# Optimization experiments

Hardware: AMD Instinct MI355X
Metric: run time of the kernel (lower is better)

The kernel has to match this reference:

```python
import jax, jax.numpy as jnp
import numpy as np

WIN = (4, 4, 4)
SHIFT = (2, 2, 2)
HEADS = 6


def _rel_index(win):
    H, W, D = win
    coords = np.stack(np.meshgrid(np.arange(H), np.arange(W), np.arange(D), indexing='ij'))
    cf = coords.reshape(3, -1)
    rel = (cf[:, :, None] - cf[:, None, :]).transpose(1, 2, 0)
    rel[..., 0] += H - 1
    rel[..., 1] += W - 1
    rel[..., 2] += D - 1
    rel[..., 0] *= (2 * W - 1) * (2 * D - 1)
    rel[..., 1] *= 2 * D - 1
    return rel.sum(-1)  # [N, N] int


def _attn_mask(shape, win, shift):
    H, W, D = shape
    wh, ww, wd = win
    mask = np.zeros((H, W, D))
    cnt = 0
    for h in (slice(0, -wh), slice(-wh, -shift[0]), slice(-shift[0], None)):
        for w in (slice(0, -ww), slice(-ww, -shift[1]), slice(-shift[1], None)):
            for d in (slice(0, -wd), slice(-wd, -shift[2]), slice(-shift[2], None)):
                mask[h, w, d] = cnt
                cnt += 1
    m = mask.reshape(H // wh, wh, W // ww, ww, D // wd, wd)
    m = m.transpose(0, 2, 4, 1, 3, 5).reshape(-1, wh * ww * wd)  # [nW, N]
    am = m[:, None, :] - m[:, :, None]
    return np.where(am != 0, -100.0, 0.0).astype(np.float32)  # [nW, N, N]


def _win_part(x, win):
    B, H, W, D, C = x.shape
    wh, ww, wd = win
    x = x.reshape(B, H // wh, wh, W // ww, ww, D // wd, wd, C)
    x = x.transpose(0, 1, 3, 5, 2, 4, 6, 7)
    return x.reshape(-1, wh * ww * wd, C)


def _win_rev(wins, win, shape):
    B, H, W, D, C = shape
    wh, ww, wd = win
    x = wins.reshape(B, H // wh, W // ww, D // wd, wh, ww, wd, C)
    x = x.transpose(0, 1, 4, 2, 5, 3, 6, 7)
    return x.reshape(B, H, W, D, C)


def _ln(x, g, b):
    m = x.mean(-1, keepdims=True)
    v = ((x - m) ** 2).mean(-1, keepdims=True)
    return (x - m) / jnp.sqrt(v + 1e-5) * g + b


def setup_inputs() -> dict:
    key = jax.random.key(0)
    ks = jax.random.split(key, 8)
    C, Hd = 192, 768
    s = 0.02
    return {
        'x': jax.random.normal(ks[0], (2, 32, 32, 32, C), jnp.float32),
        'g1': jnp.ones((C,), jnp.float32),
        'b1': jnp.zeros((C,), jnp.float32),
        'wqkv': jax.random.normal(ks[1], (C, 3 * C), jnp.float32) * s,
        'bqkv': jnp.zeros((3 * C,), jnp.float32),
        'wo': jax.random.normal(ks[2], (C, C), jnp.float32) * s,
        'bo': jnp.zeros((C,), jnp.float32),
        'bias_table': jax.random.normal(ks[3], (343, HEADS), jnp.float32) * s,
        'g2': jnp.ones((C,), jnp.float32),
        'b2': jnp.zeros((C,), jnp.float32),
        'w1': jax.random.normal(ks[4], (C, Hd), jnp.float32) * s,
        'bm1': jnp.zeros((Hd,), jnp.float32),
        'w2': jax.random.normal(ks[5], (Hd, C), jnp.float32) * s,
        'bm2': jnp.zeros((C,), jnp.float32),
    }


def reference(x, g1, b1, wqkv, bqkv, wo, bo, bias_table, g2, b2, w1, bm1, w2, bm2):
    B, H, W, D, C = x.shape
    hd = C // HEADS
    N = WIN[0] * WIN[1] * WIN[2]
    rel_idx = _rel_index(WIN)  # static numpy
    mask = jnp.asarray(_attn_mask((H, W, D), WIN, SHIFT))  # [nW, N, N]

    residual = x
    xn = _ln(x, g1, b1)
    # cyclic shift (dims divisible by window -> no padding needed)
    sx = jnp.roll(xn, (-SHIFT[0], -SHIFT[1], -SHIFT[2]), axis=(1, 2, 3))
    xw = _win_part(sx, WIN)  # [B*nW, N, C]
    B_ = xw.shape[0]
    nW = B_ // B

    qkv = (xw @ wqkv + bqkv).reshape(B_, N, 3, HEADS, hd).transpose(2, 0, 3, 1, 4)
    q, k, v = qkv[0], qkv[1], qkv[2]  # [B_, h, N, hd]
    attn = jnp.einsum('bhid,bhjd->bhij', q, k) * (hd ** -0.5)
    bias = bias_table[rel_idx.reshape(-1)].reshape(N, N, HEADS).transpose(2, 0, 1)
    attn = attn + bias[None]
    attn = attn.reshape(B, nW, HEADS, N, N) + mask[None, :, None]
    attn = jax.nn.softmax(attn.reshape(B_, HEADS, N, N), axis=-1)
    out = jnp.einsum('bhij,bhjd->bhid', attn, v).transpose(0, 2, 1, 3).reshape(B_, N, C)
    out = out @ wo + bo

    sx = _win_rev(out, WIN, (B, H, W, D, C))
    xs = jnp.roll(sx, (SHIFT[0], SHIFT[1], SHIFT[2]), axis=(1, 2, 3))
    xo = residual + xs
    h1 = jax.nn.gelu(_ln(xo, g2, b2) @ w1 + bm1, approximate=False)
    return xo + (h1 @ w2 + bm2)
```

## Files before the change

kernel.cpp:

```cpp
#include <hip/hip_runtime.h>
#include <math.h>

typedef unsigned short u16;
typedef unsigned int   u32;
using short8  = __attribute__((ext_vector_type(8))) short;
using float4v = __attribute__((ext_vector_type(4))) float;

__device__ __forceinline__ float b2f(u16 u){ return __uint_as_float(((u32)u)<<16); }
__device__ __forceinline__ u16 f2b(float f){
  u32 x = __float_as_uint(f);
  x += 0x7FFFu + ((x>>16)&1u);
  return (u16)(x>>16);
}

__device__ __forceinline__ u32 cvtpk_bf16(float lo, float hi){
  u32 r; asm("v_cvt_pk_bf16_f32 %0, %1, %2" : "=v"(r) : "v"(lo), "v"(hi));
  return r;
}

__device__ __forceinline__ void gload_lds16(const u16* g, u16* l){
  __builtin_amdgcn_global_load_lds((const __attribute__((address_space(1))) void*)g,
                                   (__attribute__((address_space(3))) void*)l, 16, 0, 0);
}

__device__ __forceinline__ float gelu_t(float x){
  float x2 = x*x;
  float z  = x * __builtin_fmaf(-0.1029434f, x2, -2.3022077f);
  float e  = __builtin_amdgcn_exp2f(z);
  return x * __builtin_amdgcn_rcpf(1.f + e);
}

__global__ void transpose_all(const float* __restrict__ wqkv, const float* __restrict__ wo,
                              const float* __restrict__ w1,   const float* __restrict__ w2,
                              const float* __restrict__ btab,
                              u16* __restrict__ wqkvT, u16* __restrict__ woT,
                              u16* __restrict__ w1P,   u16* __restrict__ w2P,
                              float* __restrict__ btabT){
  int idx = blockIdx.x*256 + threadIdx.x;
  if (idx < 110592){ int r=idx/576, c=idx-r*576; wqkvT[c*192+r]=f2b(wqkv[idx]); }
  else if (idx < 147456){ int j=idx-110592; int r=j/192, c=j-r*192; woT[c*192+r]=f2b(wo[j]); }
  else if (idx < 294912){
    int j = idx-147456;
    int tile = j >> 9, w = j & 511;
    int e = w & 7, l16 = (w>>3)&15, quad = w>>7;
    int hc = (tile/6)*16 + l16, k = (tile%6)*32 + quad*8 + e;
    w1P[j] = f2b(w1[k*768 + hc]);
  } else if (idx < 442368){
    int j = idx-294912;
    int tile = j >> 9, w = j & 511;
    int e = w & 7, l16 = (w>>3)&15, quad = w>>7;
    int oc = (tile/24)*16 + l16, k = (tile%24)*32 + quad*8 + e;
    w2P[j] = f2b(w2[k*192 + oc]);
  } else if (idx < 444426){
    int j = idx-442368;
    btabT[(j%6)*343 + j/6] = btab[j];
  }
}

__global__ __launch_bounds__(256) void ln_kernel(const float* __restrict__ x,
    const float* __restrict__ g, const float* __restrict__ bvec,
    u16* __restrict__ out)
{
  int wave = threadIdx.x >> 6, lane = threadIdx.x & 63;
  int token = blockIdx.x*4 + wave;
  int b = token >> 15, r = token & 32767;
  int hs = r >> 10, ws = (r >> 5) & 31, ds = r & 31;
  int h = (hs+2)&31, w = (ws+2)&31, d = (ds+2)&31;
  int src = ((b*32 + h)*32 + w)*32 + d;
  int win = ((b*8 + (hs>>2))*8 + (ws>>2))*8 + (ds>>2);
  int n   = ((hs&3)*4 + (ws&3))*4 + (ds&3);
  int dst = win*64 + n;
  float v[3];
  #pragma unroll
  for (int t=0;t<3;t++) v[t] = x[(size_t)src*192 + lane + t*64];
  float s  = v[0]+v[1]+v[2];
  float s2 = v[0]*v[0]+v[1]*v[1]+v[2]*v[2];
  #pragma unroll
  for (int o=32;o>=1;o>>=1){ s += __shfl_xor(s,o); s2 += __shfl_xor(s2,o); }
  float mean = s*(1.0f/192.0f);
  float var  = s2*(1.0f/192.0f) - mean*mean;
  float rstd = rsqrtf(var + 1e-5f);
  #pragma unroll
  for (int t=0;t<3;t++){
    int c = lane + t*64;
    out[(size_t)dst*192 + c] = f2b((v[t]-mean)*rstd*g[c] + bvec[c]);
  }
}

template<int MODE, int NB>
__global__ __launch_bounds__(256) void gemm_fk(
    const u16* __restrict__ A, const u16* __restrict__ BT, const float* __restrict__ bias,
    const int K, const int N,
    u16* __restrict__ outb, float* __restrict__ outf, const float* __restrict__ resf)
{
  __shared__ u16 As[64*192];
  __shared__ u16 Bs[64*192];
  const int lin = blockIdx.x;
  const int xcd = lin & 7, idx = lin >> 3;
  const int mb = idx / NB, nb = idx - mb*NB;
  const int m0 = (xcd*128 + mb) * 64, n0 = nb * 64;
  const int tid = threadIdx.x;
  const int wv = tid >> 6, lane = tid & 63;
  const int quad = lane >> 4, l16 = lane & 15;
  const int wm = (wv >> 1) * 32, wn = (wv & 1) * 32;

  float4v acc[2][2];
  #pragma unroll
  for (int a=0;a<2;a++) for (int b=0;b<2;b++) acc[a][b] = (float4v){0.f,0.f,0.f,0.f};

  const int srow8 = lane >> 3;
  const int scc   = (lane & 7) ^ srow8;
  const int c3x   = l16 & 7;

  for (int kc = 0; kc < K; kc += 192){
    #pragma unroll
    for (int t=0;t<6;t++){
      int ig = wv*6 + t;
      int g = ig >> 3, ro = ig & 7;
      int row = ro*8 + srow8;
      gload_lds16(A  + (size_t)(m0+row)*K + kc + g*64 + scc*8, As + g*4096 + ro*512);
      gload_lds16(BT + (size_t)(n0+row)*K + kc + g*64 + scc*8, Bs + g*4096 + ro*512);
    }
    __syncthreads();
    #pragma unroll
    for (int ks=0; ks<6; ks++){
      const int cc = ks*4 + quad, g = cc >> 3, c3 = (cc & 7) ^ c3x;
      short8 af[2], bf2[2];
      #pragma unroll
      for (int mt=0;mt<2;mt++) af[mt]  = *(const short8*)(As + g*4096 + (wm+mt*16+l16)*64 + c3*8);
      #pragma unroll
      for (int nt=0;nt<2;nt++) bf2[nt] = *(const short8*)(Bs + g*4096 + (wn+nt*16+l16)*64 + c3*8);
      #pragma unroll
      for (int mt=0;mt<2;mt++)
        #pragma unroll
        for (int nt=0;nt<2;nt++)
          acc[mt][nt] = __builtin_amdgcn_mfma_f32_16x16x32_bf16(af[mt], bf2[nt], acc[mt][nt], 0,0,0);
    }
    if (kc + 192 < K) __syncthreads();
  }

  #pragma unroll
  for (int nt=0;nt<2;nt++){
    int cb  = n0 + wn + nt*16;
    int col = cb + l16;
    float bv = bias[col];
    int sel  = cb / 192;
    int rem  = cb - sel*192;
    int hh   = rem >> 5, hd0 = rem & 31;
    #pragma unroll
    for (int mt=0;mt<2;mt++){
      float4v a = acc[mt][nt];
      #pragma unroll
      for (int r=0;r<4;r++){
        int mrow = m0 + wm + mt*16 + quad*4 + r;
        float v = a[r] + bv;
        if (MODE == 4){
          if (sel == 0) v *= 0.17677669529663687f;
          int win = mrow >> 6, n = mrow & 63;
          size_t dst = ((size_t)(win*6 + hh)*3 + sel)*2048 + n*32 + hd0 + l16;
          outb[dst] = f2b(v);
        } else {
          int win = mrow >> 6, n = mrow & 63;
          int b = win >> 9, rw = win & 511;
          int hs = ((rw>>6)&7)*4 + (n>>4);
          int ws = ((rw>>3)&7)*4 + ((n>>2)&3);
          int ds = (rw&7)*4 + (n&3);
          int h=(hs+2)&31, w=(ws+2)&31, d=(ds+2)&31;
          size_t t = (size_t)((b*32+h)*32+w)*32 + d;
          outf[t*192 + col] = v + resf[t*192 + col];
        }
      }
    }
  }
}

__global__ __launch_bounds__(256) void mlp_fused(
    const float* __restrict__ xo, const float* __restrict__ g2, const float* __restrict__ b2,
    const u16* __restrict__ w1P, const float* __restrict__ bm1,
    const u16* __restrict__ w2P, const float* __restrict__ bm2,
    float* __restrict__ out)
{
  __shared__ u16 S[2*32*192];
  u16* Ash = S;
  u16* Hsh = S + 32*192;
  const int tid = threadIdx.x;
  const int wv = tid >> 6, lane = tid & 63;
  const int quad = lane >> 4, l16 = lane & 15;
  const int tok0 = blockIdx.x * 32;
  const int c3x = l16 & 7;

  {
    float gg[3], bb[3];
    #pragma unroll
    for (int t=0;t<3;t++){ gg[t] = g2[lane+t*64]; bb[t] = b2[lane+t*64]; }
    #pragma unroll
    for (int tt=0;tt<8;tt++){
      const int tl = wv*8 + tt;
      const float* row = xo + (size_t)(tok0+tl)*192;
      float v[3];
      #pragma unroll
      for (int t=0;t<3;t++) v[t] = row[lane + t*64];
      float s = v[0]+v[1]+v[2];
      float s2 = v[0]*v[0]+v[1]*v[1]+v[2]*v[2];
      #pragma unroll
      for (int o=32;o>=1;o>>=1){ s += __shfl_xor(s,o); s2 += __shfl_xor(s2,o); }
      float mean = s*(1.0f/192.0f);
      float rstd = rsqrtf(s2*(1.0f/192.0f) - mean*mean + 1e-5f);
      const int slot = ((lane>>3) ^ (tl&7));
      #pragma unroll
      for (int t=0;t<3;t++)
        Ash[t*2048 + tl*64 + slot*8 + (lane&7)] = f2b((v[t]-mean)*rstd*gg[t] + bb[t]);
    }
  }
  __syncthreads();

  const int mb = wv*3;
  float4v dacc[3][2];
  #pragma unroll
  for (int a=0;a<3;a++) for (int b=0;b<2;b++) dacc[a][b] = (float4v){0.f,0.f,0.f,0.f};

  for (int p=0; p<4; p++){
    if (p) __syncthreads();
    float4v acc[3][2];
    #pragma unroll
    for (int a=0;a<3;a++) for (int b=0;b<2;b++) acc[a][b] = (float4v){0.f,0.f,0.f,0.f};
    #pragma unroll
    for (int ks=0; ks<6; ks++){
      const int cc = ks*4 + quad, g = cc >> 3, c3 = (cc & 7) ^ c3x;
      short8 bf[2], af[3];
      #pragma unroll
      for (int ntl=0;ntl<2;ntl++)
        bf[ntl] = *(const short8*)(Ash + g*2048 + (ntl*16+l16)*64 + c3*8);
      #pragma unroll
      for (int mtl=0;mtl<3;mtl++)
        af[mtl] = *(const short8*)(w1P + ((size_t)((p*12 + mb + mtl)*6 + ks)*64 + lane)*8);
      #pragma unroll
      for (int mtl=0;mtl<3;mtl++)
        #pragma unroll
        for (int ntl=0;ntl<2;ntl++)
          acc[mtl][ntl] = __builtin_amdgcn_mfma_f32_16x16x32_bf16(af[mtl], bf[ntl], acc[mtl][ntl], 0,0,0);
    }
    #pragma unroll
    for (int mtl=0;mtl<3;mtl++){
      const int hl0 = (mb+mtl)*16 + quad*4;
      const float4v bv = *(const float4v*)(bm1 + p*192 + hl0);
      const int g = hl0 >> 3, sub = hl0 & 7;
      #pragma unroll
      for (int ntl=0;ntl<2;ntl++){
        const int tok = ntl*16 + l16;
        union { unsigned long long d; u32 w[2]; } pk;
        pk.w[0] = cvtpk_bf16(gelu_t(acc[mtl][ntl][0] + bv[0]), gelu_t(acc[mtl][ntl][1] + bv[1]));
        pk.w[1] = cvtpk_bf16(gelu_t(acc[mtl][ntl][2] + bv[2]), gelu_t(acc[mtl][ntl][3] + bv[3]));
        *(unsigned long long*)(Hsh + tok*192 + ((g ^ (tok&7))<<3) + sub) = pk.d;
      }
    }
    __syncthreads();
    #pragma unroll
    for (int ks=0; ks<6; ks++){
      const int g = ks*4 + quad;
      short8 bf[2], af[3];
      #pragma unroll
      for (int ntl=0;ntl<2;ntl++){
        const int tok = ntl*16 + l16;
        bf[ntl] = *(const short8*)(Hsh + tok*192 + ((g ^ (tok&7))<<3));
      }
      #pragma unroll
      for (int mtl=0;mtl<3;mtl++)
        af[mtl] = *(const short8*)(w2P + ((size_t)((mb+mtl)*24 + p*6 + ks)*64 + lane)*8);
      #pragma unroll
      for (int mtl=0;mtl<3;mtl++)
        #pragma unroll
        for (int ntl=0;ntl<2;ntl++)
          dacc[mtl][ntl] = __builtin_amdgcn_mfma_f32_16x16x32_bf16(af[mtl], bf[ntl], dacc[mtl][ntl], 0,0,0);
    }
  }
  __syncthreads();

  float4v* F = (float4v*)S;
  #pragma unroll
  for (int mtl=0;mtl<3;mtl++){
    const int oc0 = (mb+mtl)*16 + quad*4;
    const float4v bv = *(const float4v*)(bm2 + oc0);
    #pragma unroll
    for (int ntl=0;ntl<2;ntl++){
      const int tok = ntl*16 + l16;
      float4v o;
      #pragma unroll
      for (int r=0;r<4;r++) o[r] = dacc[mtl][ntl][r] + bv[r];
      F[tok*48 + ((oc0>>2) ^ (tok&7))] = o;
    }
  }
  __syncthreads();
  const float4v* xo4 = (const float4v*)(xo + (size_t)tok0*192);
  float4v* out4 = (float4v*)(out + (size_t)tok0*192);
  #pragma unroll
  for (int it=0; it<6; it++){
    int f = it*256 + tid;
    int tok = f/48, c = f - tok*48;
    float4v v = F[tok*48 + (c ^ (tok&7))];
    float4v xv = xo4[f];
    #pragma unroll
    for (int r=0;r<4;r++) v[r] += xv[r];
    out4[f] = v;
  }
}

__global__ __launch_bounds__(192,3) void attn_mfma(
    const u16* __restrict__ qkv, const float* __restrict__ btabT,
    u16* __restrict__ out)
{
  __shared__ u16  Psh [3][64*72];
  __shared__ u16  VTsh[3][32*72];
  __shared__ float bsh[3][344];
  const int win  = blockIdx.x >> 1;
  const int wv   = threadIdx.x / 64;
  const int lane = threadIdx.x & 63;
  const int hg   = (blockIdx.x & 1)*3 + wv;
  const int quad = lane >> 4, l16 = lane & 15;

  u16* P  = &Psh[wv][0];
  u16* VT = &VTsh[wv][0];
  float* bs = &bsh[wv][0];
  const u16* base_q = qkv + ((size_t)(win*6 + hg)*3)*2048;

  for (int idx = lane; idx < 343; idx += 64) bs[idx] = btabT[hg*343 + idx];

  {
    const int a = (lane & 15)*4 + (lane >> 4);
    #pragma unroll
    for (int t=0;t<4;t++){
      union { uint4 v; u16 u[8]; } vv;
      vv.v = *(const uint4*)(base_q + 4096 + lane*32 + t*8);
      #pragma unroll
      for (int e=0;e<8;e++) VT[(t*8+e)*72 + a] = vv.u[e];
    }
  }

  short8 qf[4], kf[4];
  #pragma unroll
  for (int mt=0;mt<4;mt++) qf[mt] = *(const short8*)(base_q + (mt*16 + l16)*32 + quad*8);
  #pragma unroll
  for (int nt=0;nt<4;nt++) kf[nt] = *(const short8*)(base_q + 2048 + (nt*16 + l16)*32 + quad*8);

  float4v s[4][4];
  #pragma unroll
  for (int mt=0;mt<4;mt++)
    #pragma unroll
    for (int nt=0;nt<4;nt++)
      s[mt][nt] = __builtin_amdgcn_mfma_f32_16x16x32_bf16(qf[mt], kf[nt], (float4v){0.f,0.f,0.f,0.f}, 0,0,0);

  const int rwn = win & 511;
  const int bh=(rwn>>6)&7, bw=(rwn>>3)&7, bd=rwn&7;
  const int jw = l16>>2, jd = l16&3;
  const int gw_j = (bw==7) ? ((jw  <2)?3:6) : 0;
  const int gd_j = (bd==7) ? ((jd  <2)?1:2) : 0;
  const int gw_i = (bw==7) ? ((quad<2)?3:6) : 0;
  const int laneoff = (quad - jw)*7 - jd + 171;
  #pragma unroll
  for (int mt=0;mt<4;mt++){
    const int gh_i = (bh==7) ? ((mt<2)?9:18) : 0;
    #pragma unroll
    for (int nt=0;nt<4;nt++){
      const int gh_j = (bh==7) ? ((nt<2)?9:18) : 0;
      const int bb = (mt-nt)*49 + laneoff;
      #pragma unroll
      for (int r=0;r<4;r++){
        const int gd_i = (bd==7) ? ((r<2)?1:2) : 0;
        float sv = s[mt][nt][r] + bs[bb + r];
        if ((gh_i + gw_i + gd_i) != (gh_j + gw_j + gd_j)) sv -= 100.f;
        s[mt][nt][r] = sv;
      }
    }
  }

  #pragma unroll
  for (int mt=0;mt<4;mt++){
    #pragma unroll
    for (int r=0;r<4;r++){
      float m0 = fmaxf(fmaxf(s[mt][0][r], s[mt][1][r]), fmaxf(s[mt][2][r], s[mt][3][r]));
      #pragma unroll
      for (int o=8;o>=1;o>>=1) m0 = fmaxf(m0, __shfl_xor(m0,o));
      float sum = 0.f;
      float e[4];
      #pragma unroll
      for (int nt=0;nt<4;nt++){ e[nt] = __expf(s[mt][nt][r] - m0); sum += e[nt]; }
      #pragma unroll
      for (int o=8;o>=1;o>>=1) sum += __shfl_xor(sum,o);
      const float rinv = __builtin_amdgcn_rcpf(sum);
      union { unsigned long long d; u32 w[2]; } pk;
      pk.w[0] = cvtpk_bf16(e[0]*rinv, e[1]*rinv);
      pk.w[1] = cvtpk_bf16(e[2]*rinv, e[3]*rinv);
      *(unsigned long long*)(&P[(mt*16 + quad*4 + r)*72 + l16*4]) = pk.d;
    }
  }

  float4v o2[4][2];
  #pragma unroll
  for (int mt=0;mt<4;mt++){ o2[mt][0]=(float4v){0.f,0.f,0.f,0.f}; o2[mt][1]=(float4v){0.f,0.f,0.f,0.f}; }
  #pragma unroll
  for (int s2=0;s2<2;s2++){
    short8 vfrag[2];
    #pragma unroll
    for (int ct=0;ct<2;ct++) vfrag[ct] = *(const short8*)(&VT[(ct*16 + l16)*72 + s2*32 + quad*8]);
    #pragma unroll
    for (int mt=0;mt<4;mt++){
      short8 pfrag = *(const short8*)(&P[(mt*16 + l16)*72 + s2*32 + quad*8]);
      #pragma unroll
      for (int ct=0;ct<2;ct++)
        o2[mt][ct] = __builtin_amdgcn_mfma_f32_16x16x32_bf16(pfrag, vfrag[ct], o2[mt][ct], 0,0,0);
    }
  }

  #pragma unroll
  for (int mt=0;mt<4;mt++)
    #pragma unroll
    for (int ct=0;ct<2;ct++)
      #pragma unroll
      for (int r=0;r<4;r++){
        int i = mt*16 + quad*4 + r;
        out[((size_t)win*64 + i)*192 + hg*32 + ct*16 + l16] = f2b(o2[mt][ct][r]);
      }
}

extern "C" void kernel_launch(void* const* d_in, const int* in_sizes, int n_in,
                              void* d_out, int out_size, void* d_ws, size_t ws_size,
                              hipStream_t stream)
{
  const float* x    = (const float*)d_in[0];
  const float* g1   = (const float*)d_in[1];
  const float* b1   = (const float*)d_in[2];
  const float* wqkv = (const float*)d_in[3];
  const float* bqkv = (const float*)d_in[4];
  const float* wo   = (const float*)d_in[5];
  const float* bo   = (const float*)d_in[6];
  const float* btab = (const float*)d_in[7];
  const float* g2   = (const float*)d_in[8];
  const float* b2v  = (const float*)d_in[9];
  const float* w1   = (const float*)d_in[10];
  const float* bm1  = (const float*)d_in[11];
  const float* w2   = (const float*)d_in[12];
  const float* bm2  = (const float*)d_in[13];
  float* out = (float*)d_out;

  char* ws = (char*)d_ws;
  u16*  wqkvT = (u16*)(ws + 0);
  u16*  woT   = (u16*)(ws + 221184);
  u16*  w1P   = (u16*)(ws + 294912);
  u16*  w2P   = (u16*)(ws + 589824);
  float* btabT= (float*)(ws + 884736);
  u16*  xw    = (u16*)(ws + 1048576);
  u16*  qkvb  = (u16*)(ws + 26214400);
  float* xo   = (float*)(ws + 26214400);

  transpose_all<<<1737,256,0,stream>>>(wqkv, wo, w1, w2, btab, wqkvT, woT, w1P, w2P, btabT);

  ln_kernel<<<16384,256,0,stream>>>(x, g1, b1, xw);
  gemm_fk<4,9><<<9216,256,0,stream>>>(xw, wqkvT, bqkv, 192, 576, qkvb, nullptr, nullptr);
  attn_mfma<<<2048,192,0,stream>>>(qkvb, btabT, xw);
  gemm_fk<2,3><<<3072,256,0,stream>>>(xw, woT, bo, 192, 192, nullptr, xo, x);
  mlp_fused<<<2048,256,0,stream>>>(xo, g2, b2v, w1P, bm1, w2P, bm2, out);
}
```

Baseline: 273.1 us.

## Fuse shifted-window LayerNorm into QKV GEMM A-tile load

Removes the standalone LayerNorm kernel and computes LN1 on the fly inside the QKV GEMM. Each block gathers its 64 shifted, window-partitioned tokens from fp32 x, normalizes them, and writes bf16 directly into the swizzled LDS A tile. This saves one launch and the bf16 intermediate round-trip to memory. In exchange, every one of the 9 N-tile blocks recomputes LN for the same rows, rereading fp32 input and serializing the LN work ahead of the MFMA loop.

After: 350.5 us. +28.3%, slower.

```diff
diff --git a/kernel.cpp b/kernel.cpp
--- a/kernel.cpp
+++ b/kernel.cpp
@@ -57,41 +57,12 @@
   }
 }
 
-__global__ __launch_bounds__(256) void ln_kernel(const float* __restrict__ x,
-    const float* __restrict__ g, const float* __restrict__ bvec,
-    u16* __restrict__ out)
-{
-  int wave = threadIdx.x >> 6, lane = threadIdx.x & 63;
-  int token = blockIdx.x*4 + wave;
-  int b = token >> 15, r = token & 32767;
-  int hs = r >> 10, ws = (r >> 5) & 31, ds = r & 31;
-  int h = (hs+2)&31, w = (ws+2)&31, d = (ds+2)&31;
-  int src = ((b*32 + h)*32 + w)*32 + d;
-  int win = ((b*8 + (hs>>2))*8 + (ws>>2))*8 + (ds>>2);
-  int n   = ((hs&3)*4 + (ws&3))*4 + (ds&3);
-  int dst = win*64 + n;
-  float v[3];
-  #pragma unroll
-  for (int t=0;t<3;t++) v[t] = x[(size_t)src*192 + lane + t*64];
-  float s  = v[0]+v[1]+v[2];
-  float s2 = v[0]*v[0]+v[1]*v[1]+v[2]*v[2];
-  #pragma unroll
-  for (int o=32;o>=1;o>>=1){ s += __shfl_xor(s,o); s2 += __shfl_xor(s2,o); }
-  float mean = s*(1.0f/192.0f);
-  float var  = s2*(1.0f/192.0f) - mean*mean;
-  float rstd = rsqrtf(var + 1e-5f);
-  #pragma unroll
-  for (int t=0;t<3;t++){
-    int c = lane + t*64;
-    out[(size_t)dst*192 + c] = f2b((v[t]-mean)*rstd*g[c] + bvec[c]);
-  }
-}
-
 template<int MODE, int NB>
 __global__ __launch_bounds__(256) void gemm_fk(
     const u16* __restrict__ A, const u16* __restrict__ BT, const float* __restrict__ bias,
     const int K, const int N,
-    u16* __restrict__ outb, float* __restrict__ outf, const float* __restrict__ resf)
+    u16* __restrict__ outb, float* __restrict__ outf, const float* __restrict__ resf,
+    const float* __restrict__ lnx, const float* __restrict__ lng, const float* __restrict__ lnb)
 {
   __shared__ u16 As[64*192];
   __shared__ u16 Bs[64*192];
@@ -112,14 +83,41 @@
   const int scc   = (lane & 7) ^ srow8;
   const int c3x   = l16 & 7;
 
-  for (int kc = 0; kc < K; kc += 192){
+  if (MODE == 4){
     #pragma unroll
     for (int t=0;t<6;t++){
-      int ig = wv*6 + t;
-      int g = ig >> 3, ro = ig & 7;
-      int row = ro*8 + srow8;
-      gload_lds16(A  + (size_t)(m0+row)*K + kc + g*64 + scc*8, As + g*4096 + ro*512);
-      gload_lds16(BT + (size_t)(n0+row)*K + kc + g*64 + scc*8, Bs + g*4096 + ro*512);
+      int ig = wv*6 + t, g = ig >> 3, ro = ig & 7, row = ro*8 + srow8;
+      gload_lds16(BT + (size_t)(n0+row)*K + g*64 + scc*8, Bs + g*4096 + ro*512);
+    }
+    {
+      float gg[3], bb[3];
+      #pragma unroll
+      for (int t=0;t<3;t++){ gg[t] = lng[lane+t*64]; bb[t] = lnb[lane+t*64]; }
+      #pragma unroll
+      for (int tt=0;tt<16;tt++){
+        const int tl = wv*16 + tt;
+        const int tok = m0 + tl;
+        const int wi = tok >> 6, n = tok & 63;
+        const int b = wi >> 9, rw = wi & 511;
+        const int sh = ((rw>>6)&7)*4 + (n>>4);
+        const int sw = ((rw>>3)&7)*4 + ((n>>2)&3);
+        const int sd = (rw&7)*4 + (n&3);
+        const int h2=(sh+2)&31, w2=(sw+2)&31, d2=(sd+2)&31;
+        const float* row_p = lnx + ((size_t)((b*32+h2)*32+w2)*32 + d2)*192;
+        float v[3];
+        #pragma unroll
+        for (int t=0;t<3;t++) v[t] = row_p[lane + t*64];
+        float s  = v[0]+v[1]+v[2];
+        float s2 = v[0]*v[0]+v[1]*v[1]+v[2]*v[2];
+        #pragma unroll
+        for (int o=32;o>=1;o>>=1){ s += __shfl_xor(s,o); s2 += __shfl_xor(s2,o); }
+        float mean = s*(1.0f/192.0f);
+        float rstd = rsqrtf(s2*(1.0f/192.0f) - mean*mean + 1e-5f);
+        const int slot = ((lane>>3) ^ (tl&7));
+        #pragma unroll
+        for (int t=0;t<3;t++)
+          As[t*4096 + tl*64 + slot*8 + (lane&7)] = f2b((v[t]-mean)*rstd*gg[t] + bb[t]);
+      }
     }
     __syncthreads();
     #pragma unroll
@@ -136,32 +134,68 @@
         for (int nt=0;nt<2;nt++)
           acc[mt][nt] = __builtin_amdgcn_mfma_f32_16x16x32_bf16(af[mt], bf2[nt], acc[mt][nt], 0,0,0);
     }
-    if (kc + 192 < K) __syncthreads();
-  }
-
-  #pragma unroll
-  for (int nt=0;nt<2;nt++){
-    int cb  = n0 + wn + nt*16;
-    int col = cb + l16;
-    float bv = bias[col];
-    int sel  = cb / 192;
-    int rem  = cb - sel*192;
-    int hh   = rem >> 5, hd0 = rem & 31;
-    #pragma unroll
-    for (int mt=0;mt<2;mt++){
-      float4v a = acc[mt][nt];
-      #pragma unroll
-      for (int r=0;r<4;r++){
-        int mrow = m0 + wm + mt*16 + quad*4 + r;
-        float v = a[r] + bv;
-        if (MODE == 4){
+    #pragma unroll
+    for (int nt=0;nt<2;nt++){
+      int cb  = n0 + wn + nt*16;
+      int col = cb + l16;
+      float bv = bias[col];
+      int sel  = cb / 192;
+      int rem  = cb - sel*192;
+      int hh   = rem >> 5, hd0 = rem & 31;
+      #pragma unroll
+      for (int mt=0;mt<2;mt++){
+        float4v a = acc[mt][nt];
+        #pragma unroll
+        for (int r=0;r<4;r++){
+          int mrow = m0 + wm + mt*16 + quad*4 + r;
+          float v = a[r] + bv;
           if (sel == 0) v *= 0.17677669529663687f;
-          int win = mrow >> 6, n = mrow & 63;
-          size_t dst = ((size_t)(win*6 + hh)*3 + sel)*2048 + n*32 + hd0 + l16;
+          int wi = mrow >> 6, n = mrow & 63;
+          size_t dst = ((size_t)(wi*6 + hh)*3 + sel)*2048 + n*32 + hd0 + l16;
           outb[dst] = f2b(v);
-        } else {
-          int win = mrow >> 6, n = mrow & 63;
-          int b = win >> 9, rw = win & 511;
+        }
+      }
+    }
+  } else {
+    for (int kc = 0; kc < K; kc += 192){
+      #pragma unroll
+      for (int t=0;t<6;t++){
+        int ig = wv*6 + t;
+        int g = ig >> 3, ro = ig & 7;
+        int row = ro*8 + srow8;
+        gload_lds16(A  + (size_t)(m0+row)*K + kc + g*64 + scc*8, As + g*4096 + ro*512);
+        gload_lds16(BT + (size_t)(n0+row)*K + kc + g*64 + scc*8, Bs + g*4096 + ro*512);
+      }
+      __syncthreads();
+      #pragma unroll
+      for (int ks=0; ks<6; ks++){
+        const int cc = ks*4 + quad, g = cc >> 3, c3 = (cc & 7) ^ c3x;
+        short8 af[2], bf2[2];
+        #pragma unroll
+        for (int mt=0;mt<2;mt++) af[mt]  = *(const short8*)(As + g*4096 + (wm+mt*16+l16)*64 + c3*8);
+        #pragma unroll
+        for (int nt=0;nt<2;nt++) bf2[nt] = *(const short8*)(Bs + g*4096 + (wn+nt*16+l16)*64 + c3*8);
+        #pragma unroll
+        for (int mt=0;mt<2;mt++)
+          #pragma unroll
+          for (int nt=0;nt<2;nt++)
+            acc[mt][nt] = __builtin_amdgcn_mfma_f32_16x16x32_bf16(af[mt], bf2[nt], acc[mt][nt], 0,0,0);
+      }
+      if (kc + 192 < K) __syncthreads();
+    }
+    #pragma unroll
+    for (int nt=0;nt<2;nt++){
+      int col = n0 + wn + nt*16 + l16;
+      float bv = bias[col];
+      #pragma unroll
+      for (int mt=0;mt<2;mt++){
+        float4v a = acc[mt][nt];
+        #pragma unroll
+        for (int r=0;r<4;r++){
+          int mrow = m0 + wm + mt*16 + quad*4 + r;
+          float v = a[r] + bv;
+          int wi = mrow >> 6, n = mrow & 63;
+          int b = wi >> 9, rw = wi & 511;
           int hs = ((rw>>6)&7)*4 + (n>>4);
           int ws = ((rw>>3)&7)*4 + ((n>>2)&3);
           int ds = (rw&7)*4 + (n&3);
@@ -454,9 +488,10 @@
 
   transpose_all<<<1737,256,0,stream>>>(wqkv, wo, w1, w2, btab, wqkvT, woT, w1P, w2P, btabT);
 
-  ln_kernel<<<16384,256,0,stream>>>(x, g1, b1, xw);
-  gemm_fk<4,9><<<9216,256,0,stream>>>(xw, wqkvT, bqkv, 192, 576, qkvb, nullptr, nullptr);
+  gemm_fk<4,9><<<9216,256,0,stream>>>(nullptr, wqkvT, bqkv, 192, 576, qkvb, nullptr, nullptr,
+                                      x, g1, b1);
   attn_mfma<<<2048,192,0,stream>>>(qkvb, btabT, xw);
-  gemm_fk<2,3><<<3072,256,0,stream>>>(xw, woT, bo, 192, 192, nullptr, xo, x);
+  gemm_fk<2,3><<<3072,256,0,stream>>>(xw, woT, bo, 192, 192, nullptr, xo, x,
+                                      nullptr, nullptr, nullptr);
   mlp_fused<<<2048,256,0,stream>>>(xo, g2, b2v, w1P, bm1, w2P, bm2, out);
 }
```
